# Performance work log

Hardware: AMD Instinct MI355X
Metric: run time of the kernel (lower is better)

## Reference

```python
import jax, jax.numpy as jnp
import numpy as np

D_MODEL = 2048
D_HID = 4096
N_EXPERTS = 8
TOP_K = 2
B, S = 2, 2048


def setup_inputs() -> dict:
    key = jax.random.key(0)
    ks = jax.random.split(key, 4)
    x = jax.random.normal(ks[0], (B, S, D_MODEL), dtype=jnp.float32)
    router_w = jax.random.normal(ks[1], (D_MODEL, N_EXPERTS), dtype=jnp.float32) * (D_MODEL ** -0.5)
    w1 = jax.random.normal(ks[2], (N_EXPERTS, D_MODEL, D_HID), dtype=jnp.float32) * (D_MODEL ** -0.5)
    b1 = jnp.zeros((N_EXPERTS, D_HID), dtype=jnp.float32)
    w2 = jax.random.normal(ks[3], (N_EXPERTS, D_HID, D_MODEL), dtype=jnp.float32) * (D_HID ** -0.5)
    b2 = jnp.zeros((N_EXPERTS, D_MODEL), dtype=jnp.float32)
    return {"x": x, "router_w": router_w, "w1": w1, "b1": b1, "w2": w2, "b2": b2}


def reference(x, router_w, w1, b1, w2, b2):
    # x: [B, S, D] -> tokens [T, D]
    Bc, Sc, D = x.shape
    xt = x.reshape(-1, D)                      # [T, D]
    T = xt.shape[0]
    E = w1.shape[0]

    # --- TopKRouter: linear gate -> softmax -> top-k, renormalized weights ---
    logits = xt @ router_w                     # [T, E]
    probs = jax.nn.softmax(logits, axis=-1)    # [T, E]
    weights, indices = jax.lax.top_k(probs, TOP_K)  # [T, K]
    weights = weights / jnp.sum(weights, axis=-1, keepdims=True)

    # Combine weights per (token, expert): sum over k-slots of weight * 1[idx==e]
    combine = jnp.zeros((T, E), dtype=xt.dtype).at[
        jnp.arange(T)[:, None], indices
    ].add(weights)                             # [T, E]

    # --- Expert FFNs: Linear -> GELU (exact, torch default) -> Linear ---
    out = jnp.zeros_like(xt)
    for e in range(E):  # small fixed loop over experts
        h = jax.nn.gelu(xt @ w1[e] + b1[e], approximate=False)  # [T, H]
        y = h @ w2[e] + b2[e]                                   # [T, D]
        out = out + combine[:, e:e + 1] * y

    return out.reshape(Bc, Sc, D)
```

## Files before the change

### kernel.cpp

```cpp
#include <hip/hip_runtime.h>

typedef unsigned short u16;
typedef unsigned int u32;
typedef short bf16x8 __attribute__((ext_vector_type(8)));
typedef float f32x4 __attribute__((ext_vector_type(4)));

#define T_TOK 4096
#define DM 2048
#define DH 4096
#define NE 8
#define MAXSLOT 9216
#define MAXTILE 72

#define OFF_META   128
#define OFF_TILEE  192
#define OFF_TOPE   512
#define OFF_TOPW   33280
#define OFF_SLOTT  66048
#define OFF_UNION  102912
#define OFF_XBF    139776
#define OFF_W1T    16916992ULL
#define OFF_W2T    151134720ULL
#define OFF_Y      285352448ULL
#define OFF_H3     323101184ULL
#define NEED_Y     324149760ULL

__device__ __forceinline__ u16 f2bf(float f) {
  union { float f; u32 u; } v; v.f = f;
  u32 r = v.u + 0x7fffu + ((v.u >> 16) & 1u);
  return (u16)(r >> 16);
}

__device__ __forceinline__ float bf2f(u16 h) {
  union { u32 u; float f; } v; v.u = ((u32)h) << 16; return v.f;
}

__device__ __forceinline__ float f4c(const float4& v, int c) {
  return c == 0 ? v.x : c == 1 ? v.y : c == 2 ? v.z : v.w;
}

__device__ __forceinline__ void gl_lds16(const u16* g, u16* l) {
  typedef __attribute__((address_space(1))) const u32 gu32;
  typedef __attribute__((address_space(3))) u32 lu32;
  __builtin_amdgcn_global_load_lds((gu32*)(const void*)g, (lu32*)(void*)l, 16, 0, 0);
}

__device__ __forceinline__ float gelu_f(float v) {
  float x = v * 0.70710678118654752f;
  float ax = fabsf(x);
  float t = 1.0f / fmaf(0.3275911f, ax, 1.0f);
  float p = t * fmaf(t, fmaf(t, fmaf(t, fmaf(t, 1.061405429f, -1.453152027f),
                                     1.421413741f), -0.284496736f), 0.254829592f);
  float er = 1.0f - p * __expf(-x * x);
  er = copysignf(er, x);
  return 0.5f * v * (1.0f + er);
}

__global__ __launch_bounds__(256) void prep_kernel(
    const float* __restrict__ x, const float* __restrict__ rw,
    const float* __restrict__ w1, const float* __restrict__ w2,
    int* __restrict__ counts, int* __restrict__ top_e, float* __restrict__ top_w,
    u16* __restrict__ xbf, u16* __restrict__ w1t, u16* __restrict__ w2t)
{
  __shared__ u16 T_s[4][64][64];
  int bid = blockIdx.x;
  if (bid < 8192) {
    const float* W; u16* WtT; int N, k0, n0;
    if (bid < 4096) {
      int e = bid >> 9, r = bid & 511;
      W = w1 + (size_t)e * DM * DH;
      N = DH; k0 = (r >> 4) * 64; n0 = (r & 15) * 256;
      WtT = w1t + ((size_t)((e * 16 + (r & 15)) * 64 + (r >> 4) * 2)) * 8192;
    } else {
      int b2 = bid - 4096;
      int e = b2 >> 9, r = b2 & 511;
      W = w2 + (size_t)e * DM * DH;
      N = DM; k0 = (r >> 3) * 64; n0 = (r & 7) * 256;
      WtT = w2t + ((size_t)((e * 8 + (r & 7)) * 128 + (r >> 3) * 2)) * 8192;
    }
    int wv = threadIdx.x >> 6, l = threadIdx.x & 63;
    int nw = n0 + wv * 64;
    const float* src = W + (size_t)k0 * N + nw + l;
#pragma unroll
    for (int h = 0; h < 2; ++h) {
      float v[32];
#pragma unroll
      for (int i = 0; i < 32; ++i) v[i] = src[(size_t)(h * 32 + i) * N];
#pragma unroll
      for (int j = 0; j < 4; ++j) {
        uint4 pk;
        pk.x = f2bf(v[j * 8 + 0]) | ((u32)f2bf(v[j * 8 + 1]) << 16);
        pk.y = f2bf(v[j * 8 + 2]) | ((u32)f2bf(v[j * 8 + 3]) << 16);
        pk.z = f2bf(v[j * 8 + 4]) | ((u32)f2bf(v[j * 8 + 5]) << 16);
        pk.w = f2bf(v[j * 8 + 6]) | ((u32)f2bf(v[j * 8 + 7]) << 16);
        int slot = ((h * 4 + j) + l) & 7;
        *(uint4*)&T_s[wv][l][slot * 8] = pk;
      }
    }
    __syncthreads();
    int tid = threadIdx.x;
    int lr = tid >> 2;
    int s  = tid & 3;
    int kf = s ^ ((tid >> 3) & 3);
#pragma unroll
    for (int ks_l = 0; ks_l < 2; ++ks_l) {
      int J = ks_l * 4 + kf;
#pragma unroll
      for (int q = 0; q < 4; ++q) {
        int slot = (J + lr) & 7;
        uint4 vv = *(const uint4*)&T_s[q][lr][slot * 8];
        *(uint4*)(WtT + (size_t)ks_l * 8192 + q * 2048 + tid * 8) = vv;
      }
    }
  } else {
    int wv = threadIdx.x >> 6;
    int lane = threadIdx.x & 63;
    int t = (bid - 8192) * 4 + wv;
    const float4* xr = (const float4*)(x + (size_t)t * DM);
    const float4* rw4 = (const float4*)rw;
    float acc[NE];
#pragma unroll
    for (int e = 0; e < NE; ++e) acc[e] = 0.f;
    for (int i = 0; i < 8; ++i) {
      int d4 = i * 64 + lane;
      float4 xv = xr[d4];
      uint2 pk;
      pk.x = f2bf(xv.x) | ((u32)f2bf(xv.y) << 16);
      pk.y = f2bf(xv.z) | ((u32)f2bf(xv.w) << 16);
      *(uint2*)(xbf + (size_t)t * DM + d4 * 4) = pk;
#pragma unroll
      for (int j = 0; j < 4; ++j) {
        int d = 4 * d4 + j;
        float4 r0 = rw4[d * 2];
        float4 r1 = rw4[d * 2 + 1];
        float xs = f4c(xv, j);
        acc[0] += xs * r0.x; acc[1] += xs * r0.y; acc[2] += xs * r0.z; acc[3] += xs * r0.w;
        acc[4] += xs * r1.x; acc[5] += xs * r1.y; acc[6] += xs * r1.z; acc[7] += xs * r1.w;
      }
    }
#pragma unroll
    for (int off = 32; off > 0; off >>= 1)
#pragma unroll
      for (int e = 0; e < NE; ++e) acc[e] += __shfl_xor(acc[e], off, 64);
    if (lane == 0) {
      int e0 = 0; float l0 = acc[0];
#pragma unroll
      for (int e = 1; e < NE; ++e) if (acc[e] > l0) { l0 = acc[e]; e0 = e; }
      int e1 = -1; float l1 = -3.0e38f;
#pragma unroll
      for (int e = 0; e < NE; ++e) if (e != e0 && acc[e] > l1) { l1 = acc[e]; e1 = e; }
      float w0 = 1.f / (1.f + expf(l1 - l0));
      float w1v = 1.f - w0;
      top_e[t * 2 + 0] = e0; top_e[t * 2 + 1] = e1;
      top_w[t * 2 + 0] = w0; top_w[t * 2 + 1] = w1v;
      atomicAdd(&counts[e0], 1);
      atomicAdd(&counts[e1], 1);
    }
  }
}

__global__ void scan_kernel(int* __restrict__ wsI)
{
  int* counts = wsI;
  int* curs   = wsI + 8;
  int* offs   = wsI + 16;
  int* meta   = wsI + (OFF_META / 4);
  int* tile_e = wsI + (OFF_TILEE / 4);
  int* slot_token = wsI + (OFF_SLOTT / 4);
  float* slot_wt = (float*)(wsI + (OFF_UNION / 4));
  __shared__ int s_off[9];
  if (threadIdx.x == 0) {
    int o = 0;
    for (int e = 0; e < NE; ++e) {
      offs[e] = o; curs[e] = o; s_off[e] = o;
      o += (counts[e] + 127) & ~127;
    }
    offs[8] = o; s_off[8] = o;
    meta[0] = o >> 7;
  }
  __syncthreads();
  int nt = s_off[8] >> 7;
  for (int i = threadIdx.x; i < MAXTILE; i += blockDim.x) {
    int e = -1;
    if (i < nt) {
      for (int j = 0; j < NE; ++j)
        if (i * 128 >= s_off[j] && i * 128 < s_off[j + 1]) e = j;
    }
    tile_e[i] = e;
  }
  for (int i = threadIdx.x; i < MAXSLOT; i += blockDim.x) {
    slot_token[i] = -1;
    slot_wt[i] = 0.f;
  }
}

__global__ void scatter_kernel(const int* __restrict__ top_e, const float* __restrict__ top_w,
                               int* __restrict__ curs, int* __restrict__ slot_token,
                               int* __restrict__ tok_slots, float* __restrict__ slot_wt,
                               int useY)
{
  int t = blockIdx.x * blockDim.x + threadIdx.x;
  if (t >= T_TOK) return;
#pragma unroll
  for (int k = 0; k < 2; ++k) {
    int e = top_e[t * 2 + k];
    int pos = atomicAdd(&curs[e], 1);
    slot_token[pos] = t;
    if (useY) tok_slots[t * 2 + k] = pos;
    else      slot_wt[pos] = top_w[t * 2 + k];
  }
}


#define GATEN(n) asm volatile("s_waitcnt vmcnt(" #n ")" ::: "memory")
#define NOGATE ((void)0)
#define NOSTG  ((void)0)
#define NORD   ((void)0)

#define SA_(PA, KO) do { \
  gl_lds16(aptr0 + (KO), &PA[wid * 16][0]);        \
  gl_lds16(aptr1 + (KO), &PA[64 + wid * 16][0]); } while (0)
#define SBALL(PB, KS) do { \
  gl_lds16(bptrT + (size_t)(KS) * 8192,        &PB[wid * 16][0]);        \
  gl_lds16(bptrT + (size_t)(KS) * 8192 + 2048, &PB[64 + wid * 16][0]);   \
  gl_lds16(bptrT + (size_t)(KS) * 8192 + 4096, &PB[128 + wid * 16][0]);  \
  gl_lds16(bptrT + (size_t)(KS) * 8192 + 6144, &PB[192 + wid * 16][0]); } while (0)

#define RDAF8(P)                                                        \
  _Pragma("unroll")                                                     \
  for (int i_ = 0; i_ < 8; ++i_)                                        \
    af[i_] = *(const bf16x8*)&P[i_ * 16 + lrow][sp8]
#define RDBF(P)                                                         \
  _Pragma("unroll")                                                     \
  for (int n_ = 0; n_ < 4; ++n_)                                        \
    bfr[n_] = *(const bf16x8*)&P[wn + n_ * 16 + lrow][sp8]

#define PHF(STG, GATE, RD) do {                                         \
  STG;                                                                  \
  GATE;                                                                 \
  __builtin_amdgcn_s_barrier();                                         \
  asm volatile("s_waitcnt lgkmcnt(0)" ::: "memory");                    \
  __builtin_amdgcn_sched_barrier(0);                                    \
  __builtin_amdgcn_s_setprio(1);                                        \
  _Pragma("unroll")                                                     \
  for (int nf = 0; nf < 4; ++nf)                                        \
    _Pragma("unroll")                                                   \
    for (int mf = 0; mf < 8; ++mf)                                      \
      acc[nf][mf] = __builtin_amdgcn_mfma_f32_16x16x32_bf16(            \
          bfr[nf], af[mf], acc[nf][mf], 0, 0, 0);                       \
  __builtin_amdgcn_s_setprio(0);                                        \
  RD;                                                                   \
  __builtin_amdgcn_s_barrier();                                         \
  __builtin_amdgcn_sched_barrier(0);                                    \
} while (0)

template<int MODE, int EPI>
__global__ __launch_bounds__(256, 2) void gemm_tb(
    const u16* __restrict__ Wt, const float* __restrict__ bias,
    const u16* __restrict__ Abase,
    u16* __restrict__ Hout, u16* __restrict__ Ybuf, float* __restrict__ Out,
    const int* __restrict__ slot_token, const float* __restrict__ slot_wt,
    const int* __restrict__ tile_e, const int* __restrict__ meta,
    int tile0, int mtc)
{
  constexpr int KD = (MODE == 0) ? DM : DH;
  constexpr int ND = (MODE == 0) ? DH : DM;
  constexpr int NT = ND / 256;
  constexpr int NK = KD / 32;

  __shared__ u16 A_s[3][128][32];
  __shared__ u16 B_s[3][256][32];

  int nwg = gridDim.x;
  int flat = blockIdx.x;
  int q8 = nwg >> 3, rr = nwg & 7;
  int xcd = flat & 7, i0 = flat >> 3;
  int wg = (xcd < rr ? xcd * (q8 + 1) : rr * (q8 + 1) + (xcd - rr) * q8) + i0;
  int mloc = wg / NT;
  int ntile = wg % NT;
  int mt = tile0 + mloc;
  if (mt >= meta[0]) return;
  int e = tile_e[mt];
  int n0 = ntile * 256;

  const int tid = threadIdx.x;
  const int lane = tid & 63;
  const int wid = tid >> 6;
  const int lrow = lane & 15;
  const int g = lane >> 4;
  const int sp8 = (g ^ ((lrow >> 1) & 3)) << 3;
  const int wn = wid << 6;

  const int srow = tid >> 2;
  const int swz = ((tid & 3) ^ ((tid >> 3) & 3)) << 3;

  const u16 *aptr0, *aptr1;
  if (MODE == 0) {
    int t0 = slot_token[mt * 128 + srow];       if (t0 < 0) t0 = 0;
    int t1 = slot_token[mt * 128 + 64 + srow];  if (t1 < 0) t1 = 0;
    aptr0 = Abase + (size_t)t0 * KD + swz;
    aptr1 = Abase + (size_t)t1 * KD + swz;
  } else {
    aptr0 = Abase + (size_t)(mloc * 128 + srow) * KD + swz;
    aptr1 = Abase + (size_t)(mloc * 128 + 64 + srow) * KD + swz;
  }
  const u16* bptrT = Wt + ((size_t)(e * NT + ntile) * NK) * 8192 + tid * 8;

  f32x4 acc[4][8] = {};
  bf16x8 af[8], bfr[4];

  u16 (*pA0)[32] = A_s[0]; u16 (*pA1)[32] = A_s[1]; u16 (*pA2)[32] = A_s[2];
  u16 (*pB0)[32] = B_s[0]; u16 (*pB1)[32] = B_s[1]; u16 (*pB2)[32] = B_s[2];

  SA_(pA0, 0); SBALL(pB0, 0);
  SA_(pA1, 32); SBALL(pB1, 1);
  GATEN(6);
  __builtin_amdgcn_s_barrier();
  __builtin_amdgcn_sched_barrier(0);
  RDAF8(pA0);
  RDBF(pB0);

  for (int t = 0; t < NK - 2; ++t) {
    int ko = (t + 2) * 32;
    PHF(SA_(pA2, ko); SBALL(pB2, t + 2), GATEN(6),
        RDAF8(pA1); RDBF(pB1));
    u16 (*tA)[32] = pA0; pA0 = pA1; pA1 = pA2; pA2 = tA;
    u16 (*tB)[32] = pB0; pB0 = pB1; pB1 = pB2; pB2 = tB;
  }
  PHF(NOSTG, GATEN(0), RDAF8(pA1); RDBF(pB1));
  PHF(NOSTG, NOGATE, NORD);

  const int rb = g << 2;
  float4 bias4[4];
#pragma unroll
  for (int nf = 0; nf < 4; ++nf)
    bias4[nf] = *(const float4*)&bias[e * ND + n0 + wn + nf * 16 + rb];

  if constexpr (MODE == 0) {
#pragma unroll
    for (int mf = 0; mf < 8; ++mf) {
      u16* hp = Hout + (size_t)(mloc * 128 + mf * 16 + lrow) * DH + n0 + wn + rb;
#pragma unroll
      for (int nf = 0; nf < 4; ++nf) {
        float v0 = gelu_f(acc[nf][mf][0] + bias4[nf].x);
        float v1 = gelu_f(acc[nf][mf][1] + bias4[nf].y);
        float v2 = gelu_f(acc[nf][mf][2] + bias4[nf].z);
        float v3 = gelu_f(acc[nf][mf][3] + bias4[nf].w);
        uint2 pk;
        pk.x = f2bf(v0) | ((u32)f2bf(v1) << 16);
        pk.y = f2bf(v2) | ((u32)f2bf(v3) << 16);
        *(uint2*)(hp + nf * 16) = pk;
      }
    }
  } else if constexpr (EPI == 0) {
#pragma unroll
    for (int mf = 0; mf < 8; ++mf) {
      u16* yp = Ybuf + (size_t)(mt * 128 + mf * 16 + lrow) * DM + n0 + wn + rb;
#pragma unroll
      for (int nf = 0; nf < 4; ++nf) {
        float v0 = acc[nf][mf][0] + bias4[nf].x;
        float v1 = acc[nf][mf][1] + bias4[nf].y;
        float v2 = acc[nf][mf][2] + bias4[nf].z;
        float v3 = acc[nf][mf][3] + bias4[nf].w;
        uint2 pk;
        pk.x = f2bf(v0) | ((u32)f2bf(v1) << 16);
        pk.y = f2bf(v2) | ((u32)f2bf(v3) << 16);
        *(uint2*)(yp + nf * 16) = pk;
      }
    }
  } else {
#pragma unroll
    for (int mf = 0; mf < 8; ++mf) {
      int gs = mt * 128 + mf * 16 + lrow;
      int tok = slot_token[gs];
      if (tok < 0) continue;
      float wt = slot_wt[gs];
      float* op = Out + (size_t)tok * DM + n0 + wn + rb;
#pragma unroll
      for (int nf = 0; nf < 4; ++nf) {
        atomicAdd(op + nf * 16 + 0, wt * (acc[nf][mf][0] + bias4[nf].x));
        atomicAdd(op + nf * 16 + 1, wt * (acc[nf][mf][1] + bias4[nf].y));
        atomicAdd(op + nf * 16 + 2, wt * (acc[nf][mf][2] + bias4[nf].z));
        atomicAdd(op + nf * 16 + 3, wt * (acc[nf][mf][3] + bias4[nf].w));
      }
    }
  }
}

__global__ __launch_bounds__(256) void combine_kernel(
    const u16* __restrict__ y, const int* __restrict__ tok_slots,
    const float* __restrict__ top_w, float* __restrict__ out)
{
  int t = blockIdx.x;
  int d = threadIdx.x * 8;
  int s0 = tok_slots[t * 2], s1 = tok_slots[t * 2 + 1];
  float w0 = top_w[t * 2], w1 = top_w[t * 2 + 1];
  union { uint4 u; u16 s[8]; } a, b;
  a.u = *(const uint4*)(y + (size_t)s0 * DM + d);
  b.u = *(const uint4*)(y + (size_t)s1 * DM + d);
  float o[8];
#pragma unroll
  for (int j = 0; j < 8; ++j) o[j] = w0 * bf2f(a.s[j]) + w1 * bf2f(b.s[j]);
  float* op = out + (size_t)t * DM + d;
  *(float4*)op = make_float4(o[0], o[1], o[2], o[3]);
  *(float4*)(op + 4) = make_float4(o[4], o[5], o[6], o[7]);
}

extern "C" void kernel_launch(void* const* d_in, const int* in_sizes, int n_in,
                              void* d_out, int out_size, void* d_ws, size_t ws_size,
                              hipStream_t stream) {
  const float* x  = (const float*)d_in[0];
  const float* rw = (const float*)d_in[1];
  const float* w1 = (const float*)d_in[2];
  const float* b1 = (const float*)d_in[3];
  const float* w2 = (const float*)d_in[4];
  const float* b2 = (const float*)d_in[5];
  float* out = (float*)d_out;
  char* ws = (char*)d_ws;

  int* counts = (int*)ws;
  int* curs   = (int*)(ws + 32);
  int* meta   = (int*)(ws + OFF_META);
  int* tile_e = (int*)(ws + OFF_TILEE);
  int* top_e  = (int*)(ws + OFF_TOPE);
  float* top_w = (float*)(ws + OFF_TOPW);
  int* slot_token = (int*)(ws + OFF_SLOTT);
  int* tok_slots  = (int*)(ws + OFF_UNION);
  float* slot_wt  = (float*)(ws + OFF_UNION);
  u16* xbf = (u16*)(ws + OFF_XBF);
  u16* w1t = (u16*)(ws + OFF_W1T);
  u16* w2t = (u16*)(ws + OFF_W2T);

  const int useY = (ws_size >= NEED_Y) ? 1 : 0;
  u16* ybuf = (u16*)(ws + OFF_Y);
  u16* hbuf = (u16*)(ws + (useY ? OFF_H3 : OFF_Y));

  hipMemsetAsync(ws, 0, 512, stream);
  if (!useY) hipMemsetAsync(d_out, 0, (size_t)out_size * sizeof(float), stream);

  prep_kernel<<<9216, 256, 0, stream>>>(x, rw, w1, w2, counts, top_e, top_w,
                                        xbf, w1t, w2t);
  scan_kernel<<<1, 256, 0, stream>>>((int*)ws);
  scatter_kernel<<<T_TOK / 256, 256, 0, stream>>>(top_e, top_w, curs, slot_token,
                                                  tok_slots, slot_wt, useY);

  size_t hoff = useY ? OFF_H3 : OFF_Y;
  size_t avail = ws_size > hoff ? ws_size - hoff : (size_t)DH * 256;
  long ch_slots = (long)(avail / (DH * 2));
  ch_slots = (ch_slots / 128) * 128;
  if (ch_slots > MAXSLOT) ch_slots = MAXSLOT;
  if (ch_slots < 128) ch_slots = 128;
  int mtc = (int)(ch_slots / 128);
  int nchunks = (MAXTILE + mtc - 1) / mtc;

  for (int c = 0; c < nchunks; ++c) {
    int tile0 = c * mtc;
    gemm_tb<0, 0><<<dim3(mtc * (DH / 256)), 256, 0, stream>>>(
        w1t, b1, xbf, hbuf, nullptr, nullptr, slot_token, slot_wt, tile_e, meta, tile0, mtc);
    if (useY) {
      gemm_tb<1, 0><<<dim3(mtc * (DM / 256)), 256, 0, stream>>>(
          w2t, b2, hbuf, nullptr, ybuf, nullptr, slot_token, slot_wt, tile_e, meta, tile0, mtc);
    } else {
      gemm_tb<1, 1><<<dim3(mtc * (DM / 256)), 256, 0, stream>>>(
          w2t, b2, hbuf, nullptr, nullptr, out, slot_token, slot_wt, tile_e, meta, tile0, mtc);
    }
  }
  if (useY)
    combine_kernel<<<T_TOK, 256, 0, stream>>>(ybuf, tok_slots, top_w, out);
}
```

Before: 671.4 us.

## Overlap W2 bf16 conversion with first-chunk GEMM1 by interleaving workgroups

The conversion and transposition of W2 from fp32 to bf16 moves out of the prep kernel and into the first GEMM1 launch as extra workgroups, spread evenly among the GEMM tiles by an index mapping. This is meant to hide the memory-bound W2 conversion behind the compute-bound GEMM1 and to shorten the serial prep phase. The cost is more complex block remapping that can disturb the XCD-aware tile placement. The W2 workgroups also contend with GEMM blocks for bandwidth and CU slots.

New measurement: 738.5 us. 10.0% more time.

```diff
diff --git a/kernel.cpp b/kernel.cpp
--- a/kernel.cpp
+++ b/kernel.cpp
@@ -58,26 +58,17 @@
 
 __global__ __launch_bounds__(256) void prep_kernel(
     const float* __restrict__ x, const float* __restrict__ rw,
-    const float* __restrict__ w1, const float* __restrict__ w2,
+    const float* __restrict__ w1,
     int* __restrict__ counts, int* __restrict__ top_e, float* __restrict__ top_w,
-    u16* __restrict__ xbf, u16* __restrict__ w1t, u16* __restrict__ w2t)
+    u16* __restrict__ xbf, u16* __restrict__ w1t)
 {
   __shared__ u16 T_s[4][64][64];
   int bid = blockIdx.x;
-  if (bid < 8192) {
-    const float* W; u16* WtT; int N, k0, n0;
-    if (bid < 4096) {
-      int e = bid >> 9, r = bid & 511;
-      W = w1 + (size_t)e * DM * DH;
-      N = DH; k0 = (r >> 4) * 64; n0 = (r & 15) * 256;
-      WtT = w1t + ((size_t)((e * 16 + (r & 15)) * 64 + (r >> 4) * 2)) * 8192;
-    } else {
-      int b2 = bid - 4096;
-      int e = b2 >> 9, r = b2 & 511;
-      W = w2 + (size_t)e * DM * DH;
-      N = DM; k0 = (r >> 3) * 64; n0 = (r & 7) * 256;
-      WtT = w2t + ((size_t)((e * 8 + (r & 7)) * 128 + (r >> 3) * 2)) * 8192;
-    }
+  if (bid < 4096) {
+    int e = bid >> 9, r = bid & 511;
+    const float* W = w1 + (size_t)e * DM * DH;
+    int N = DH, k0 = (r >> 4) * 64, n0 = (r & 15) * 256;
+    u16* WtT = w1t + ((size_t)((e * 16 + (r & 15)) * 64 + (r >> 4) * 2)) * 8192;
     int wv = threadIdx.x >> 6, l = threadIdx.x & 63;
     int nw = n0 + wv * 64;
     const float* src = W + (size_t)k0 * N + nw + l;
@@ -115,7 +106,7 @@
   } else {
     int wv = threadIdx.x >> 6;
     int lane = threadIdx.x & 63;
-    int t = (bid - 8192) * 4 + wv;
+    int t = (bid - 4096) * 4 + wv;
     const float4* xr = (const float4*)(x + (size_t)t * DM);
     const float4* rw4 = (const float4*)rw;
     float acc[NE];
@@ -261,7 +252,8 @@
     u16* __restrict__ Hout, u16* __restrict__ Ybuf, float* __restrict__ Out,
     const int* __restrict__ slot_token, const float* __restrict__ slot_wt,
     const int* __restrict__ tile_e, const int* __restrict__ meta,
-    int tile0, int mtc)
+    int tile0, int mtc,
+    const float* __restrict__ W2src, u16* __restrict__ W2dst, int nw2)
 {
   constexpr int KD = (MODE == 0) ? DM : DH;
   constexpr int ND = (MODE == 0) ? DH : DM;
@@ -271,8 +263,59 @@
   __shared__ u16 A_s[3][128][32];
   __shared__ u16 B_s[3][256][32];
 
-  int nwg = gridDim.x;
   int flat = blockIdx.x;
+  int nwg = gridDim.x - nw2;
+
+  if (MODE == 0 && nw2 > 0) {
+    unsigned long long G = (unsigned long long)gridDim.x;
+    unsigned long long c0 = ((unsigned long long)flat * (unsigned long long)nwg) / G;
+    unsigned long long c1 = (((unsigned long long)flat + 1ull) * (unsigned long long)nwg) / G;
+    if (c1 == c0) {
+      int ti = flat - (int)c0;
+      u16 (*T_s)[64] = (u16 (*)[64])&B_s[0][0][0];
+      int e = ti >> 9, r = ti & 511;
+      const float* W = W2src + (size_t)e * DM * DH;
+      int N = DM, k0 = (r >> 3) * 64, n0 = (r & 7) * 256;
+      u16* WtT = W2dst + ((size_t)((e * 8 + (r & 7)) * 128 + (r >> 3) * 2)) * 8192;
+      int wv = threadIdx.x >> 6, l = threadIdx.x & 63;
+      int nw_ = n0 + wv * 64;
+      const float* src = W + (size_t)k0 * N + nw_ + l;
+#pragma unroll
+      for (int h = 0; h < 2; ++h) {
+        float v[32];
+#pragma unroll
+        for (int i = 0; i < 32; ++i) v[i] = src[(size_t)(h * 32 + i) * N];
+#pragma unroll
+        for (int j = 0; j < 4; ++j) {
+          uint4 pk;
+          pk.x = f2bf(v[j * 8 + 0]) | ((u32)f2bf(v[j * 8 + 1]) << 16);
+          pk.y = f2bf(v[j * 8 + 2]) | ((u32)f2bf(v[j * 8 + 3]) << 16);
+          pk.z = f2bf(v[j * 8 + 4]) | ((u32)f2bf(v[j * 8 + 5]) << 16);
+          pk.w = f2bf(v[j * 8 + 6]) | ((u32)f2bf(v[j * 8 + 7]) << 16);
+          int slot = ((h * 4 + j) + l) & 7;
+          *(uint4*)&T_s[wv * 64 + l][slot * 8] = pk;
+        }
+      }
+      __syncthreads();
+      int tid_ = threadIdx.x;
+      int lr = tid_ >> 2;
+      int s  = tid_ & 3;
+      int kf = s ^ ((tid_ >> 3) & 3);
+#pragma unroll
+      for (int ks_l = 0; ks_l < 2; ++ks_l) {
+        int J = ks_l * 4 + kf;
+#pragma unroll
+        for (int q = 0; q < 4; ++q) {
+          int slot = (J + lr) & 7;
+          uint4 vv = *(const uint4*)&T_s[q * 64 + lr][slot * 8];
+          *(uint4*)(WtT + (size_t)ks_l * 8192 + q * 2048 + tid_ * 8) = vv;
+        }
+      }
+      return;
+    }
+    flat = (int)c0;
+  }
+
   int q8 = nwg >> 3, rr = nwg & 7;
   int xcd = flat & 7, i0 = flat >> 3;
   int wg = (xcd < rr ? xcd * (q8 + 1) : rr * (q8 + 1) + (xcd - rr) * q8) + i0;
@@ -438,8 +481,7 @@
   hipMemsetAsync(ws, 0, 512, stream);
   if (!useY) hipMemsetAsync(d_out, 0, (size_t)out_size * sizeof(float), stream);
 
-  prep_kernel<<<9216, 256, 0, stream>>>(x, rw, w1, w2, counts, top_e, top_w,
-                                        xbf, w1t, w2t);
+  prep_kernel<<<5120, 256, 0, stream>>>(x, rw, w1, counts, top_e, top_w, xbf, w1t);
   scan_kernel<<<1, 256, 0, stream>>>((int*)ws);
   scatter_kernel<<<T_TOK / 256, 256, 0, stream>>>(top_e, top_w, curs, slot_token,
                                                   tok_slots, slot_wt, useY);
@@ -455,14 +497,18 @@
 
   for (int c = 0; c < nchunks; ++c) {
     int tile0 = c * mtc;
-    gemm_tb<0, 0><<<dim3(mtc * (DH / 256)), 256, 0, stream>>>(
-        w1t, b1, xbf, hbuf, nullptr, nullptr, slot_token, slot_wt, tile_e, meta, tile0, mtc);
+    int nw2 = (c == 0) ? 4096 : 0;
+    gemm_tb<0, 0><<<dim3(mtc * (DH / 256) + nw2), 256, 0, stream>>>(
+        w1t, b1, xbf, hbuf, nullptr, nullptr, slot_token, slot_wt, tile_e, meta,
+        tile0, mtc, w2, w2t, nw2);
     if (useY) {
       gemm_tb<1, 0><<<dim3(mtc * (DM / 256)), 256, 0, stream>>>(
-          w2t, b2, hbuf, nullptr, ybuf, nullptr, slot_token, slot_wt, tile_e, meta, tile0, mtc);
+          w2t, b2, hbuf, nullptr, ybuf, nullptr, slot_token, slot_wt, tile_e, meta,
+          tile0, mtc, nullptr, nullptr, 0);
     } else {
       gemm_tb<1, 1><<<dim3(mtc * (DM / 256)), 256, 0, stream>>>(
-          w2t, b2, hbuf, nullptr, nullptr, out, slot_token, slot_wt, tile_e, meta, tile0, mtc);
+          w2t, b2, hbuf, nullptr, nullptr, out, slot_token, slot_wt, tile_e, meta,
+          tile0, mtc, nullptr, nullptr, 0);
     }
   }
   if (useY)
```
